# Kernel optimization log

Hardware: AMD Instinct MI355X
Metric: run time of the kernel (lower is better)

The kernel has to match this reference:

```python
import jax, jax.numpy as jnp
import numpy as np

NUM_EXPERTS = 64


def setup_inputs() -> dict:
    key = jax.random.key(0)
    k1, k2 = jax.random.split(key)
    x = jax.random.normal(k1, (8192, 4096), dtype=jnp.float32)
    W = jax.random.normal(k2, (NUM_EXPERTS, 4096), dtype=jnp.float32) * 0.02
    return {"x": x, "W": W}


def reference(x, W):
    # gate: logits = x @ W^T  -> [T, E]
    logits = jnp.einsum('th,eh->te', x, W)
    scores = jax.nn.softmax(logits, axis=-1)
    # top_k == 1 path: max with keepdim (torch scores.max(dim=-1, keepdim=True))
    expert_weights = jnp.max(scores, axis=-1, keepdims=True)      # [T, 1]
    expert_indices = jnp.argmax(scores, axis=-1, keepdims=True)   # [T, 1] int
    # routing_counts = bincount(expert_indices.squeeze(1), minlength=E)
    routing_counts = jnp.bincount(expert_indices[:, 0], length=NUM_EXPERTS)
    return (expert_weights, expert_indices, scores, routing_counts)
```

## Files before the change

### kernel.cpp

```cpp
#include <hip/hip_runtime.h>
#include <stdint.h>

#define T_TOKENS 8192
#define K_DIM    4096
#define NEXP     64
#define TB       128
#define KC       64

typedef short bf16x8 __attribute__((ext_vector_type(8)));
typedef float f32x4  __attribute__((ext_vector_type(4)));

__device__ __forceinline__ uint32_t f2bf(float v) {
    uint32_t u = __builtin_bit_cast(uint32_t, v);
    return (u + 0x7fffu + ((u >> 16) & 1u)) >> 16;
}
__device__ __forceinline__ float bf2f(uint32_t b) {
    return __builtin_bit_cast(float, b << 16);
}
struct S3 { short h, l, q; };
__device__ __forceinline__ S3 cvt1(float v) {
    uint32_t hb = f2bf(v); float r  = v - bf2f(hb);
    uint32_t lb = f2bf(r); float r2 = r - bf2f(lb);
    uint32_t qb = f2bf(r2);
    S3 o; o.h = (short)hb; o.l = (short)lb; o.q = (short)qb; return o;
}
__device__ __forceinline__ void cvt8(const float4 a0, const float4 a1,
                                     bf16x8& xh, bf16x8& xl, bf16x8& xq) {
    const float av[8] = {a0.x, a0.y, a0.z, a0.w, a1.x, a1.y, a1.z, a1.w};
#pragma unroll
    for (int j = 0; j < 8; ++j) {
        S3 o = cvt1(av[j]);
        xh[j] = o.h; xl[j] = o.l; xq[j] = o.q;
    }
}

__global__ void wpack(const float* __restrict__ W, float4* __restrict__ Wf,
                      float* __restrict__ out_counts) {
    const int l     = threadIdx.x;
    const int kstep = blockIdx.x;
    const int etile = blockIdx.y;
    if (kstep == 0 && etile == 0)
        out_counts[l] = 0.f;
    const int e = etile * 16 + (l & 15);
    const int k = kstep * 32 + (l >> 4) * 8;
    const float* src = W + (size_t)e * K_DIM + k;
    bf16x8 h, l1, l2;
#pragma unroll
    for (int j = 0; j < 8; ++j) {
        S3 o = cvt1(src[j]);
        h[j] = o.h; l1[j] = o.l; l2[j] = o.q;
    }
    const size_t base = ((size_t)(kstep * 4 + etile) * 3) * 64 + l;
    Wf[base]       = __builtin_bit_cast(float4, h);
    Wf[base + 64]  = __builtin_bit_cast(float4, l1);
    Wf[base + 128] = __builtin_bit_cast(float4, l2);
}

template <int NCH>
__global__ __launch_bounds__(512, 4) void gemm_mfma(
    const float*  __restrict__ x,
    const float4* __restrict__ Wf,
    float* __restrict__ P)
{
    static_assert(NCH >= 4, "pipeline needs >=4 chunks");
    __shared__ float4 bbuf[2][1536];

    const int tid  = threadIdx.x;
    const int l    = tid & 63;
    const int wv   = __builtin_amdgcn_readfirstlane(tid >> 6);
    const int t0   = blockIdx.x * TB;
    const int slice = blockIdx.y;
    const int k0   = slice * (NCH * KC);

    const float4* x4 = (const float4*)x;
    const int arow = wv * 16 + (l & 15);
    const size_t xg = (size_t)(t0 + arow) * (K_DIM / 4) + (size_t)(k0 >> 2) + ((l >> 4) * 2);
    const size_t bg0 = ((size_t)(k0 >> 5)) * 768;

    f32x4 acc[4];
#pragma unroll
    for (int et = 0; et < 4; ++et) acc[et] = (f32x4){0.f, 0.f, 0.f, 0.f};

#pragma unroll
    for (int q = 0; q < 3; ++q)
        __builtin_amdgcn_global_load_lds(
            (const __attribute__((address_space(1))) void*)(Wf + bg0 + (wv * 3 + q) * 64 + l),
            (__attribute__((address_space(3))) void*)&bbuf[0][(wv * 3 + q) * 64],
            16, 0, 0);
    __builtin_amdgcn_sched_barrier(0);
    float4 xa0 = x4[xg + 0], xa1 = x4[xg + 1];
    float4 xa2 = x4[xg + 8], xa3 = x4[xg + 9];
    __builtin_amdgcn_sched_barrier(0);
    float4 xn0 = x4[xg + 16], xn1 = x4[xg + 17];
    float4 xn2 = x4[xg + 24], xn3 = x4[xg + 25];
    __builtin_amdgcn_sched_barrier(0);

#pragma unroll
    for (int c = 0; c < NCH; ++c) {
        const int b  = c & 1;
        const int nb = b ^ 1;

        if (c + 1 < NCH) {
            const size_t bo = bg0 + (size_t)(c + 1) * 1536;
#pragma unroll
            for (int q = 0; q < 3; ++q)
                __builtin_amdgcn_global_load_lds(
                    (const __attribute__((address_space(1))) void*)(Wf + bo + (wv * 3 + q) * 64 + l),
                    (__attribute__((address_space(3))) void*)&bbuf[nb][(wv * 3 + q) * 64],
                    16, 0, 0);
        }
        __builtin_amdgcn_sched_barrier(0);
        float4 xm0 = xn0, xm1 = xn1, xm2 = xn2, xm3 = xn3;
        if (c + 2 < NCH) {
            const size_t xo = xg + (size_t)(c + 2) * 16;
            xm0 = x4[xo + 0]; xm1 = x4[xo + 1];
            xm2 = x4[xo + 8]; xm3 = x4[xo + 9];
        }
        __builtin_amdgcn_sched_barrier(0);

        if (c + 2 < NCH)      asm volatile("s_waitcnt vmcnt(11)" ::: "memory");
        else if (c + 1 < NCH) asm volatile("s_waitcnt vmcnt(7)"  ::: "memory");
        else                  asm volatile("s_waitcnt vmcnt(0)"  ::: "memory");
        __builtin_amdgcn_s_barrier();

        bf16x8 xh0, xl0, xq0, xh1, xl1, xq1;
        cvt8(xa0, xa1, xh0, xl0, xq0);
        cvt8(xa2, xa3, xh1, xl1, xq1);

#pragma unroll
        for (int et = 0; et < 4; ++et) {
            {
                const float4* bp = &bbuf[b][et * 192 + l];
                bf16x8 wh = __builtin_bit_cast(bf16x8, bp[0]);
                bf16x8 wl = __builtin_bit_cast(bf16x8, bp[64]);
                bf16x8 wq = __builtin_bit_cast(bf16x8, bp[128]);
                acc[et] = __builtin_amdgcn_mfma_f32_16x16x32_bf16(xh0, wh, acc[et], 0, 0, 0);
                acc[et] = __builtin_amdgcn_mfma_f32_16x16x32_bf16(xh0, wl, acc[et], 0, 0, 0);
                acc[et] = __builtin_amdgcn_mfma_f32_16x16x32_bf16(xh0, wq, acc[et], 0, 0, 0);
                acc[et] = __builtin_amdgcn_mfma_f32_16x16x32_bf16(xl0, wh, acc[et], 0, 0, 0);
                acc[et] = __builtin_amdgcn_mfma_f32_16x16x32_bf16(xl0, wl, acc[et], 0, 0, 0);
                acc[et] = __builtin_amdgcn_mfma_f32_16x16x32_bf16(xq0, wh, acc[et], 0, 0, 0);
            }
            {
                const float4* bp = &bbuf[b][768 + et * 192 + l];
                bf16x8 wh = __builtin_bit_cast(bf16x8, bp[0]);
                bf16x8 wl = __builtin_bit_cast(bf16x8, bp[64]);
                bf16x8 wq = __builtin_bit_cast(bf16x8, bp[128]);
                acc[et] = __builtin_amdgcn_mfma_f32_16x16x32_bf16(xh1, wh, acc[et], 0, 0, 0);
                acc[et] = __builtin_amdgcn_mfma_f32_16x16x32_bf16(xh1, wl, acc[et], 0, 0, 0);
                acc[et] = __builtin_amdgcn_mfma_f32_16x16x32_bf16(xh1, wq, acc[et], 0, 0, 0);
                acc[et] = __builtin_amdgcn_mfma_f32_16x16x32_bf16(xl1, wh, acc[et], 0, 0, 0);
                acc[et] = __builtin_amdgcn_mfma_f32_16x16x32_bf16(xl1, wl, acc[et], 0, 0, 0);
                acc[et] = __builtin_amdgcn_mfma_f32_16x16x32_bf16(xq1, wh, acc[et], 0, 0, 0);
            }
        }

        asm volatile("s_waitcnt lgkmcnt(0)" ::: "memory");
        __builtin_amdgcn_sched_barrier(0);
        __builtin_amdgcn_s_barrier();

        xa0 = xn0; xa1 = xn1; xa2 = xn2; xa3 = xn3;
        xn0 = xm0; xn1 = xm1; xn2 = xm2; xn3 = xm3;
    }

    float* Pp = P + (size_t)slice * T_TOKENS * NEXP;
#pragma unroll
    for (int et = 0; et < 4; ++et) {
#pragma unroll
        for (int i = 0; i < 4; ++i) {
            int t = t0 + wv * 16 + (l >> 4) * 4 + i;
            Pp[(size_t)t * NEXP + et * 16 + (l & 15)] = acc[et][i];
        }
    }
}

template <int S>
__global__ __launch_bounds__(256) void router_finish_t(
    const float* __restrict__ P, float* __restrict__ out)
{
    const int lane = threadIdx.x & 63;
    const int wv   = threadIdx.x >> 6;
    const int t    = blockIdx.x * 4 + wv;

    float lg = 0.f;
#pragma unroll
    for (int s = 0; s < S; ++s)
        lg += P[((size_t)s * T_TOKENS + t) * NEXP + lane];

    float* out_w = out;
    float* out_i = out + T_TOKENS;
    float* out_s = out + 2 * T_TOKENS;
    float* out_c = out + 2 * T_TOKENS + (size_t)T_TOKENS * NEXP;

    float m = lg;
#pragma unroll
    for (int off = 32; off > 0; off >>= 1)
        m = fmaxf(m, __shfl_xor(m, off));
    float p = expf(lg - m);
    float s = p;
#pragma unroll
    for (int off = 32; off > 0; off >>= 1)
        s += __shfl_xor(s, off);
    float sc = p / s;

    float bv = sc; int bi = lane;
#pragma unroll
    for (int off = 32; off > 0; off >>= 1) {
        float ov = __shfl_xor(bv, off);
        int   oi = __shfl_xor(bi, off);
        if (ov > bv || (ov == bv && oi < bi)) { bv = ov; bi = oi; }
    }
    out_s[(size_t)t * NEXP + lane] = sc;
    if (lane == 0) {
        out_w[t] = bv;
        out_i[t] = (float)bi;
        atomicAdd(&out_c[bi], 1.0f);
    }
}

extern "C" void kernel_launch(void* const* d_in, const int* in_sizes, int n_in,
                              void* d_out, int out_size, void* d_ws, size_t ws_size,
                              hipStream_t stream)
{
    const float* x = (const float*)d_in[0];
    const float* W = (const float*)d_in[1];
    float* out = (float*)d_out;
    float* out_s = out + 2 * T_TOKENS;
    float* out_c = out + 2 * T_TOKENS + (size_t)T_TOKENS * NEXP;

    const size_t wf_bytes  = (size_t)128 * 4 * 3 * 64 * 16;
    const size_t per_slice = (size_t)T_TOKENS * NEXP * sizeof(float);

    int S = 8;
    while (S > 1 && wf_bytes + (size_t)S * per_slice > ws_size) S >>= 1;
    float4* Wf = (float4*)d_ws;
    float* Pbuf;
    if (wf_bytes + per_slice <= ws_size) {
        Pbuf = (float*)((char*)d_ws + wf_bytes);
    } else {
        S = 1;
        Pbuf = out_s;
    }

    wpack<<<dim3(128, 4), 64, 0, stream>>>(W, Wf, out_c);
    switch (S) {
        case 8: gemm_mfma<8> <<<dim3(T_TOKENS / TB, 8), 512, 0, stream>>>(x, Wf, Pbuf); break;
        case 4: gemm_mfma<16><<<dim3(T_TOKENS / TB, 4), 512, 0, stream>>>(x, Wf, Pbuf); break;
        case 2: gemm_mfma<32><<<dim3(T_TOKENS / TB, 2), 512, 0, stream>>>(x, Wf, Pbuf); break;
        default: gemm_mfma<64><<<dim3(T_TOKENS / TB, 1), 512, 0, stream>>>(x, Wf, Pbuf); break;
    }
    switch (S) {
        case 8: router_finish_t<8><<<T_TOKENS / 4, 256, 0, stream>>>(Pbuf, out); break;
        case 4: router_finish_t<4><<<T_TOKENS / 4, 256, 0, stream>>>(Pbuf, out); break;
        case 2: router_finish_t<2><<<T_TOKENS / 4, 256, 0, stream>>>(Pbuf, out); break;
        default: router_finish_t<1><<<T_TOKENS / 4, 256, 0, stream>>>(Pbuf, out); break;
    }
}
```

Before: 98.20 us.

## Stage x tiles through LDS via async global_load_lds with XOR swizzle

Activation tiles are now fetched with direct global-to-LDS async loads into a swizzled, double-buffered shared buffer, replacing the register-prefetch pipeline. Each wave then reads its fragments from LDS, and the loop is simplified to one barrier pair per chunk. The K-split count drops from 8 to 4 and the occupancy hint from 4 to 2, which halves the partial-sum buffer traffic but gives fewer blocks. The extra 64KB of LDS per block limits residency, and the loop is no longer unrolled.

```diff
diff --git a/kernel.cpp b/kernel.cpp
--- a/kernel.cpp
+++ b/kernel.cpp
@@ -33,6 +33,11 @@
         xh[j] = o.h; xl[j] = o.l; xq[j] = o.q;
     }
 }
+
+#define GLDS(srcp, dstp) \
+    __builtin_amdgcn_global_load_lds( \
+        (const __attribute__((address_space(1))) void*)(srcp), \
+        (__attribute__((address_space(3))) void*)(dstp), 16, 0, 0)
 
 __global__ void wpack(const float* __restrict__ W, float4* __restrict__ Wf,
                       float* __restrict__ out_counts) {
@@ -57,12 +62,12 @@
 }
 
 template <int NCH>
-__global__ __launch_bounds__(512, 4) void gemm_mfma(
+__global__ __launch_bounds__(512, 2) void gemm_mfma(
     const float*  __restrict__ x,
     const float4* __restrict__ Wf,
     float* __restrict__ P)
 {
-    static_assert(NCH >= 4, "pipeline needs >=4 chunks");
+    __shared__ float4 xbuf[2][2048];
     __shared__ float4 bbuf[2][1536];
 
     const int tid  = threadIdx.x;
@@ -73,59 +78,62 @@
     const int k0   = slice * (NCH * KC);
 
     const float4* x4 = (const float4*)x;
-    const int arow = wv * 16 + (l & 15);
-    const size_t xg = (size_t)(t0 + arow) * (K_DIM / 4) + (size_t)(k0 >> 2) + ((l >> 4) * 2);
+    const int rsub = wv * 4 + (l >> 4);
+    const int colx = (l & 15) ^ (rsub & 7);
+    size_t xsrc[4];
+#pragma unroll
+    for (int q = 0; q < 4; ++q)
+        xsrc[q] = ((size_t)(t0 + q * 32 + rsub) << 10) + (size_t)(k0 >> 2) + colx;
+
     const size_t bg0 = ((size_t)(k0 >> 5)) * 768;
 
     f32x4 acc[4];
 #pragma unroll
     for (int et = 0; et < 4; ++et) acc[et] = (f32x4){0.f, 0.f, 0.f, 0.f};
 
+    const int r  = wv * 16 + (l & 15);
+    const int sb = (l >> 4) * 2;
+    const int rx = r & 7;
+    const int ia0 = r * 16 + ((sb + 0) ^ rx);
+    const int ia1 = r * 16 + ((sb + 1) ^ rx);
+    const int ia2 = r * 16 + ((sb + 8) ^ rx);
+    const int ia3 = r * 16 + ((sb + 9) ^ rx);
+
 #pragma unroll
     for (int q = 0; q < 3; ++q)
-        __builtin_amdgcn_global_load_lds(
-            (const __attribute__((address_space(1))) void*)(Wf + bg0 + (wv * 3 + q) * 64 + l),
-            (__attribute__((address_space(3))) void*)&bbuf[0][(wv * 3 + q) * 64],
-            16, 0, 0);
-    __builtin_amdgcn_sched_barrier(0);
-    float4 xa0 = x4[xg + 0], xa1 = x4[xg + 1];
-    float4 xa2 = x4[xg + 8], xa3 = x4[xg + 9];
-    __builtin_amdgcn_sched_barrier(0);
-    float4 xn0 = x4[xg + 16], xn1 = x4[xg + 17];
-    float4 xn2 = x4[xg + 24], xn3 = x4[xg + 25];
-    __builtin_amdgcn_sched_barrier(0);
-
-#pragma unroll
+        GLDS(Wf + bg0 + (wv * 3 + q) * 64 + l, &bbuf[0][(wv * 3 + q) * 64]);
+#pragma unroll
+    for (int q = 0; q < 4; ++q)
+        GLDS(x4 + xsrc[q], &xbuf[0][q * 512 + wv * 64]);
+
     for (int c = 0; c < NCH; ++c) {
         const int b  = c & 1;
         const int nb = b ^ 1;
 
+        __builtin_amdgcn_s_barrier();
+
         if (c + 1 < NCH) {
             const size_t bo = bg0 + (size_t)(c + 1) * 1536;
 #pragma unroll
             for (int q = 0; q < 3; ++q)
-                __builtin_amdgcn_global_load_lds(
-                    (const __attribute__((address_space(1))) void*)(Wf + bo + (wv * 3 + q) * 64 + l),
-                    (__attribute__((address_space(3))) void*)&bbuf[nb][(wv * 3 + q) * 64],
-                    16, 0, 0);
+                GLDS(Wf + bo + (wv * 3 + q) * 64 + l, &bbuf[nb][(wv * 3 + q) * 64]);
+            const size_t xo = (size_t)(c + 1) * 16;
+#pragma unroll
+            for (int q = 0; q < 4; ++q)
+                GLDS(x4 + xsrc[q] + xo, &xbuf[nb][q * 512 + wv * 64]);
+            asm volatile("s_waitcnt vmcnt(7)" ::: "memory");
+        } else {
+            asm volatile("s_waitcnt vmcnt(0)" ::: "memory");
         }
-        __builtin_amdgcn_sched_barrier(0);
-        float4 xm0 = xn0, xm1 = xn1, xm2 = xn2, xm3 = xn3;
-        if (c + 2 < NCH) {
-            const size_t xo = xg + (size_t)(c + 2) * 16;
-            xm0 = x4[xo + 0]; xm1 = x4[xo + 1];
-            xm2 = x4[xo + 8]; xm3 = x4[xo + 9];
-        }
-        __builtin_amdgcn_sched_barrier(0);
-
-        if (c + 2 < NCH)      asm volatile("s_waitcnt vmcnt(11)" ::: "memory");
-        else if (c + 1 < NCH) asm volatile("s_waitcnt vmcnt(7)"  ::: "memory");
-        else                  asm volatile("s_waitcnt vmcnt(0)"  ::: "memory");
         __builtin_amdgcn_s_barrier();
 
+        float4 a0 = xbuf[b][ia0];
+        float4 a1 = xbuf[b][ia1];
+        float4 a2 = xbuf[b][ia2];
+        float4 a3 = xbuf[b][ia3];
         bf16x8 xh0, xl0, xq0, xh1, xl1, xq1;
-        cvt8(xa0, xa1, xh0, xl0, xq0);
-        cvt8(xa2, xa3, xh1, xl1, xq1);
+        cvt8(a0, a1, xh0, xl0, xq0);
+        cvt8(a2, a3, xh1, xl1, xq1);
 
 #pragma unroll
         for (int et = 0; et < 4; ++et) {
@@ -154,13 +162,6 @@
                 acc[et] = __builtin_amdgcn_mfma_f32_16x16x32_bf16(xq1, wh, acc[et], 0, 0, 0);
             }
         }
-
-        asm volatile("s_waitcnt lgkmcnt(0)" ::: "memory");
-        __builtin_amdgcn_sched_barrier(0);
-        __builtin_amdgcn_s_barrier();
-
-        xa0 = xn0; xa1 = xn1; xa2 = xn2; xa3 = xn3;
-        xn0 = xm0; xn1 = xm1; xn2 = xm2; xn3 = xm3;
     }
 
     float* Pp = P + (size_t)slice * T_TOKENS * NEXP;
@@ -231,7 +232,7 @@
     const size_t wf_bytes  = (size_t)128 * 4 * 3 * 64 * 16;
     const size_t per_slice = (size_t)T_TOKENS * NEXP * sizeof(float);
 
-    int S = 8;
+    int S = 4;
     while (S > 1 && wf_bytes + (size_t)S * per_slice > ws_size) S >>= 1;
     float4* Wf = (float4*)d_ws;
     float* Pbuf;
@@ -244,13 +245,11 @@
 
     wpack<<<dim3(128, 4), 64, 0, stream>>>(W, Wf, out_c);
     switch (S) {
-        case 8: gemm_mfma<8> <<<dim3(T_TOKENS / TB, 8), 512, 0, stream>>>(x, Wf, Pbuf); break;
         case 4: gemm_mfma<16><<<dim3(T_TOKENS / TB, 4), 512, 0, stream>>>(x, Wf, Pbuf); break;
         case 2: gemm_mfma<32><<<dim3(T_TOKENS / TB, 2), 512, 0, stream>>>(x, Wf, Pbuf); break;
         default: gemm_mfma<64><<<dim3(T_TOKENS / TB, 1), 512, 0, stream>>>(x, Wf, Pbuf); break;
     }
     switch (S) {
-        case 8: router_finish_t<8><<<T_TOKENS / 4, 256, 0, stream>>>(Pbuf, out); break;
         case 4: router_finish_t<4><<<T_TOKENS / 4, 256, 0, stream>>>(Pbuf, out); break;
         case 2: router_finish_t<2><<<T_TOKENS / 4, 256, 0, stream>>>(Pbuf, out); break;
         default: router_finish_t<1><<<T_TOKENS / 4, 256, 0, stream>>>(Pbuf, out); break;
```

Result: no change. 98.44 us (+0.2%).
